# Kernel tuning notes

Measured on AMD Instinct MI355X. Metric: run time of the kernel, lower is better.

The kernel has to match this reference:

```python
import jax, jax.numpy as jnp
import numpy as np

NUM_GROUPS = 32
EPS = 1e-5


def group_norm(x, scale, bias):
    # x: [B, C, L], normalize per (group, batch) over (C//G, L)
    B, C, L = x.shape
    G = NUM_GROUPS
    xg = x.reshape(B, G, C // G, L)
    mean = xg.mean(axis=(2, 3), keepdims=True)
    var = xg.var(axis=(2, 3), keepdims=True)
    xg = (xg - mean) * jax.lax.rsqrt(var + EPS)
    h = xg.reshape(B, C, L)
    return h * scale[None, :, None] + bias[None, :, None]


def setup_inputs() -> dict:
    key = jax.random.key(0)
    ks = jax.random.split(key, 8)
    B, C, L = 8, 512, 2048
    s = 1.0 / np.sqrt(C)
    return {
        "x": jax.random.normal(ks[0], (B, C, L), jnp.float32),
        "gn_scale": jnp.ones((C,), jnp.float32),
        "gn_bias": jnp.zeros((C,), jnp.float32),
        "wq": jax.random.normal(ks[1], (C, C), jnp.float32) * s,
        "bq": jnp.zeros((C,), jnp.float32),
        "wk": jax.random.normal(ks[2], (C, C), jnp.float32) * s,
        "bk": jnp.zeros((C,), jnp.float32),
        "wv": jax.random.normal(ks[3], (C, C), jnp.float32) * s,
        "bv": jnp.zeros((C,), jnp.float32),
        "wo": jax.random.normal(ks[4], (C, C), jnp.float32) * s,
        "bo": jnp.zeros((C,), jnp.float32),
    }


def reference(x, gn_scale, gn_bias, wq, bq, wk, bk, wv, bv, wo, bo):
    B, C, L = x.shape
    h = group_norm(x, gn_scale, gn_bias)  # [B, C, L]
    # 1x1 conv == per-position linear; produce [B, L, C] directly
    q = jnp.einsum('oc,bcl->blo', wq, h) + bq
    k = jnp.einsum('oc,bcl->blo', wk, h) + bk
    v = jnp.einsum('oc,bcl->blo', wv, h) + bv
    scale = jnp.asarray(C, x.dtype) ** -0.5
    w = jnp.einsum('bqc,bkc->bqk', q, k) * scale  # [B, L, L]
    w = jax.nn.softmax(w, axis=-1)
    a = jnp.einsum('bqk,bkc->bqc', w, v)  # [B, L, C]
    out = jnp.einsum('oc,blc->bol', wo, a) + bo[None, :, None]  # [B, C, L]
    return x + out
```

## Files before the change

kernel.cpp:

```cpp
#include <hip/hip_runtime.h>

typedef __attribute__((ext_vector_type(8))) _Float16 half8;
typedef __attribute__((ext_vector_type(4))) _Float16 half4;
typedef __attribute__((ext_vector_type(4))) float floatx4;

#define AS1 __attribute__((address_space(1)))
#define AS3 __attribute__((address_space(3)))

__device__ __forceinline__ void async_load16(const void* g, void* l) {
  __builtin_amdgcn_global_load_lds((AS1 void*)(unsigned long long)g,
                                   (AS3 void*)(unsigned long long)l, 16, 0, 0);
}

template <int N>
__device__ __forceinline__ void wait_vm() {
  static_assert(N >= 0 && N <= 12, "extend wait_vm");
  if constexpr (N == 0) asm volatile("s_waitcnt vmcnt(0)" ::: "memory");
  else if constexpr (N == 1) asm volatile("s_waitcnt vmcnt(1)" ::: "memory");
  else if constexpr (N == 2) asm volatile("s_waitcnt vmcnt(2)" ::: "memory");
  else if constexpr (N == 3) asm volatile("s_waitcnt vmcnt(3)" ::: "memory");
  else if constexpr (N == 4) asm volatile("s_waitcnt vmcnt(4)" ::: "memory");
  else if constexpr (N == 5) asm volatile("s_waitcnt vmcnt(5)" ::: "memory");
  else if constexpr (N == 6) asm volatile("s_waitcnt vmcnt(6)" ::: "memory");
  else if constexpr (N == 7) asm volatile("s_waitcnt vmcnt(7)" ::: "memory");
  else if constexpr (N == 8) asm volatile("s_waitcnt vmcnt(8)" ::: "memory");
  else if constexpr (N == 9) asm volatile("s_waitcnt vmcnt(9)" ::: "memory");
  else if constexpr (N == 10) asm volatile("s_waitcnt vmcnt(10)" ::: "memory");
  else if constexpr (N == 11) asm volatile("s_waitcnt vmcnt(11)" ::: "memory");
  else asm volatile("s_waitcnt vmcnt(12)" ::: "memory");
}

__global__ __launch_bounds__(256) void gn_fused(const float* __restrict__ x,
                                                const float* __restrict__ gsc,
                                                const float* __restrict__ gbi,
                                                _Float16* __restrict__ ht) {
  constexpr int STR = 2056;
  __shared__ _Float16 xl[16 * STR];
  __shared__ float rs[4], rss[4], mv[2], scs[16], ofs[16];
  const int bg = blockIdx.x;
  const int b = bg >> 5, g = bg & 31;
  const float4* p4 = (const float4*)(x + (long long)bg * 32768);
  const int t = threadIdx.x;
  float s = 0.f, ss = 0.f;
  for (int i = t; i < 8192; i += 256) {
    float4 v = p4[i];
    const int c = i >> 9, lq = (i & 511) << 2;
    half4 pk;
    pk[0] = (_Float16)v.x; pk[1] = (_Float16)v.y;
    pk[2] = (_Float16)v.z; pk[3] = (_Float16)v.w;
    *(half4*)&xl[c * STR + lq] = pk;
    s += v.x + v.y + v.z + v.w;
    ss += v.x * v.x + v.y * v.y + v.z * v.z + v.w * v.w;
  }
#pragma unroll
  for (int off = 32; off; off >>= 1) { s += __shfl_down(s, off); ss += __shfl_down(ss, off); }
  if ((t & 63) == 0) { rs[t >> 6] = s; rss[t >> 6] = ss; }
  __syncthreads();
  if (t == 0) {
    s = rs[0] + rs[1] + rs[2] + rs[3];
    ss = rss[0] + rss[1] + rss[2] + rss[3];
    float mean = s * (1.f / 32768.f);
    float var = ss * (1.f / 32768.f) - mean * mean;
    mv[0] = mean; mv[1] = rsqrtf(var + 1e-5f);
  }
  __syncthreads();
  if (t < 16) {
    const float sc = gsc[g * 16 + t] * mv[1];
    scs[t] = sc;
    ofs[t] = gbi[g * 16 + t] - mv[0] * sc;
  }
  __syncthreads();
  const int l0 = t * 8;
  half8 hv[16];
#pragma unroll
  for (int c = 0; c < 16; ++c) hv[c] = *(const half8*)&xl[c * STR + l0];
  _Float16* dst0 = ht + ((long long)(b * 2048 + l0)) * 512 + g * 16;
#pragma unroll
  for (int j = 0; j < 8; ++j) {
    half8 o0, o1;
#pragma unroll
    for (int c = 0; c < 8; ++c) o0[c] = (_Float16)((float)hv[c][j] * scs[c] + ofs[c]);
#pragma unroll
    for (int c = 0; c < 8; ++c) o1[c] = (_Float16)((float)hv[c + 8][j] * scs[c + 8] + ofs[c + 8]);
    _Float16* dst = dst0 + (long long)j * 512;
    *(half8*)dst = o0;
    *(half8*)(dst + 8) = o1;
  }
}

__global__ __launch_bounds__(256) void cast_w(const float* __restrict__ w0, const float* __restrict__ w1,
                                              const float* __restrict__ w2, const float* __restrict__ w3,
                                              const float* __restrict__ bq, const float* __restrict__ bk,
                                              _Float16* __restrict__ outw, float* __restrict__ bqk) {
  const long long i = (long long)blockIdx.x * 256 + threadIdx.x;
  if (blockIdx.x < 4096) {
    const int m = (int)(i >> 18);
    const int r = (int)(i & 262143);
    const float* w = (m == 0) ? w0 : (m == 1) ? w1 : (m == 2) ? w2 : w3;
    outw[i] = (_Float16)w[r];
  } else {
    const int j = (int)(i - 4096LL * 256);
    bqk[j] = (j < 512) ? bq[j] : bk[j - 512];
  }
}

template <int BM, int BN, int BIAS_MODE , int OUT_TYPE , bool RESIDUAL>
__global__ __launch_bounds__(512, 2) void gemm2p(
    const _Float16* __restrict__ A, long long sA, int lda,
    const _Float16* __restrict__ Bt, long long sB, int ldb,
    void* __restrict__ Cv, long long sC, int ldc,
    const float* __restrict__ bias,
    const float* __restrict__ resid, long long sR,
    float alpha, int K) {
  constexpr int ASZ = BM * 64, BSZ = BN * 64;
  constexpr int BUF = ASZ + BSZ;
  constexpr int RWA = BM / 16, RWB = BN / 16;
  constexpr int LA = RWA / 8, LB = RWB / 8;
  constexpr int L = 2 * LA + 2 * LB;
  constexpr int NMI = BM / 64, NNJ = BN / 128;
  __shared__ __align__(16) _Float16 ls[2 * BUF];

  const int tid = threadIdx.x;
  const int wave = tid >> 6, lane = tid & 63;
  const int wr = wave >> 2, wc = wave & 3;
  const int fm = lane & 15, q = lane >> 4;
  const int bz = blockIdx.x;
  const int m0 = blockIdx.y * BM, n0 = blockIdx.z * BN;
  A += (long long)bz * sA;
  Bt += (long long)bz * sB;

  const int srow = lane >> 3;
  const int schunk = ((lane & 7) ^ (srow & 7)) * 8;
  const _Float16* pA0 = A + (long long)(m0 + RWA * wave + srow) * lda + schunk;
  const _Float16* pA1 = pA0 + (long long)(BM / 2) * lda;
  const _Float16* pB0 = Bt + (long long)(n0 + RWB * wave + srow) * ldb + schunk;
  const _Float16* pB1 = pB0 + (long long)(BN / 2) * ldb;
  const int dA0 = RWA * wave * 64;
  const int dB0 = ASZ + RWB * wave * 64;

  const int c0 = (q ^ (fm & 7)) * 8;
  const int c1 = ((q + 4) ^ (fm & 7)) * 8;
  const int arow = wr * (BM / 4) + fm;
  const int brow = wc * (BN / 8) + fm;

  floatx4 acc[2][2][NMI][NNJ] = {};
  half8 af[NMI][2], bf0[NNJ][2], bf1[NNJ][2];

  const int NT = K >> 6;

  {
    _Float16* st = ls;
#pragma unroll
    for (int s = 0; s < LA; ++s) async_load16(pA0 + (long long)(8 * s) * lda, st + dA0 + s * 512);
#pragma unroll
    for (int s = 0; s < LB; ++s) async_load16(pB0 + (long long)(8 * s) * ldb, st + dB0 + s * 512);
#pragma unroll
    for (int s = 0; s < LB; ++s) async_load16(pB1 + (long long)(8 * s) * ldb, st + dB0 + BSZ / 2 + s * 512);
#pragma unroll
    for (int s = 0; s < LA; ++s) async_load16(pA1 + (long long)(8 * s) * lda, st + dA0 + ASZ / 2 + s * 512);
    pA0 += 64; pA1 += 64; pB0 += 64; pB1 += 64;
    wait_vm<0>();
  }

#define G8_READ_A(MH)                                                      \
  _Pragma("unroll") for (int mi = 0; mi < NMI; ++mi) {                     \
    const int r_ = (MH) * (BM / 2) + arow + 16 * mi;                       \
    af[mi][0] = *(const half8*)&cb[r_ * 64 + c0];                          \
    af[mi][1] = *(const half8*)&cb[r_ * 64 + c1];                          \
  }
#define G8_READ_B(NH, BF)                                                  \
  _Pragma("unroll") for (int nj = 0; nj < NNJ; ++nj) {                     \
    const int r_ = ASZ + ((NH) * (BN / 2) + brow + 16 * nj) * 64;          \
    BF[nj][0] = *(const half8*)&cb[r_ + c0];                               \
    BF[nj][1] = *(const half8*)&cb[r_ + c1];                               \
  }
#define G8_MFMA(MH, NH, BF)                                                \
  __builtin_amdgcn_s_setprio(1);                                           \
  _Pragma("unroll") for (int kk = 0; kk < 2; ++kk)                         \
  _Pragma("unroll") for (int mi = 0; mi < NMI; ++mi)                       \
  _Pragma("unroll") for (int nj = 0; nj < NNJ; ++nj)                       \
    acc[MH][NH][mi][nj] = __builtin_amdgcn_mfma_f32_16x16x32_f16(          \
        af[mi][kk], BF[nj][kk], acc[MH][NH][mi][nj], 0, 0, 0);             \
  __builtin_amdgcn_s_setprio(0);
#define G8_STAGE_A(PTR, OFF)                                               \
  _Pragma("unroll") for (int s = 0; s < LA; ++s)                           \
    async_load16(PTR + (long long)(8 * s) * lda, st + dA0 + (OFF) + s * 512);
#define G8_STAGE_B(PTR, OFF)                                               \
  _Pragma("unroll") for (int s = 0; s < LB; ++s)                           \
    async_load16(PTR + (long long)(8 * s) * ldb, st + dB0 + (OFF) + s * 512);

  for (int kt = 0; kt < NT - 1; ++kt) {
    const _Float16* cb = ls + (kt & 1) * BUF;
    _Float16* st = ls + ((kt + 1) & 1) * BUF;
    __builtin_amdgcn_s_barrier();
    G8_READ_A(0)
    G8_READ_B(0, bf0)
    G8_READ_B(1, bf1)
    G8_STAGE_A(pA0, 0)
    G8_STAGE_B(pB0, 0)
    G8_STAGE_B(pB1, BSZ / 2)
    G8_STAGE_A(pA1, ASZ / 2)
    pA0 += 64; pA1 += 64; pB0 += 64; pB1 += 64;
    wait_vm<L>();
    G8_MFMA(0, 0, bf0)
    G8_MFMA(0, 1, bf1)
    __builtin_amdgcn_s_barrier();
    G8_READ_A(1)
    wait_vm<LA>();
    G8_MFMA(1, 1, bf1)
    G8_MFMA(1, 0, bf0)
  }
  {
    const _Float16* cb = ls + ((NT - 1) & 1) * BUF;
    __builtin_amdgcn_s_barrier();
    G8_READ_A(0)
    G8_READ_B(0, bf0)
    G8_READ_B(1, bf1)
    wait_vm<0>();
    G8_MFMA(0, 0, bf0)
    G8_MFMA(0, 1, bf1)
    __builtin_amdgcn_s_barrier();
    G8_READ_A(1)
    G8_MFMA(1, 1, bf1)
    G8_MFMA(1, 0, bf0)
  }

#undef G8_READ_A
#undef G8_READ_B
#undef G8_MFMA
#undef G8_STAGE_A
#undef G8_STAGE_B

#pragma unroll
  for (int mh = 0; mh < 2; ++mh)
#pragma unroll
    for (int nh = 0; nh < 2; ++nh)
#pragma unroll
      for (int mi = 0; mi < NMI; ++mi)
#pragma unroll
        for (int nj = 0; nj < NNJ; ++nj) {
          const int rr0 = m0 + mh * (BM / 2) + wr * (BM / 4) + 16 * mi + 4 * q;
          const int cc = n0 + nh * (BN / 2) + wc * (BN / 8) + 16 * nj + fm;
#pragma unroll
          for (int t = 0; t < 4; ++t) {
            const int rr = rr0 + t;
            float v = acc[mh][nh][mi][nj][t] * alpha;
            if (BIAS_MODE == 1) v += bias[cc];
            if (BIAS_MODE == 2) v += bias[rr];
            if (RESIDUAL) v += resid[(long long)bz * sR + (long long)rr * ldc + cc];
            const long long off = (long long)bz * sC + (long long)rr * ldc + cc;
            if (OUT_TYPE == 0) ((float*)Cv)[off] = v;
            else ((_Float16*)Cv)[off] = (_Float16)v;
          }
        }
}

__global__ __launch_bounds__(256) void row_stats(const _Float16* __restrict__ S,
                                                 float2* __restrict__ rms) {
  const int row = blockIdx.x * 4 + (threadIdx.x >> 6);
  const int lane = threadIdx.x & 63;
  const float4* p4 = (const float4*)(S + (long long)row * 2048);
  union U { float4 f; _Float16 h[8]; } u[4];
#pragma unroll
  for (int j = 0; j < 4; ++j) u[j].f = p4[lane + 64 * j];
  float v[32];
  float mx = -3e38f;
#pragma unroll
  for (int j = 0; j < 4; ++j)
#pragma unroll
    for (int i = 0; i < 8; ++i) { v[j * 8 + i] = (float)u[j].h[i]; mx = fmaxf(mx, v[j * 8 + i]); }
#pragma unroll
  for (int off = 32; off; off >>= 1) mx = fmaxf(mx, __shfl_xor(mx, off));
  float s = 0.f;
#pragma unroll
  for (int i = 0; i < 32; ++i) s += __expf(v[i] - mx);
#pragma unroll
  for (int off = 32; off; off >>= 1) s += __shfl_xor(s, off);
  if (lane == 0) rms[row] = make_float2(mx, 1.f / s);
}

__global__ __launch_bounds__(512, 2) void gemm_pv(
    const _Float16* __restrict__ S, const float2* __restrict__ rms,
    const _Float16* __restrict__ Vt, _Float16* __restrict__ Out) {
  constexpr int BM = 128, BN = 256;
  constexpr int ASZ = BM * 64, BSZ = BN * 64, BUF = ASZ + BSZ;
  constexpr int LB = 2;
  constexpr int NMI = 2, NNJ = 2;
  constexpr int NT = 32;
  __shared__ __align__(16) _Float16 ls[2 * BUF];

  const int tid = threadIdx.x;
  const int wave = tid >> 6, lane = tid & 63;
  const int wr = wave >> 2, wc = wave & 3;
  const int fm = lane & 15, q = lane >> 4;
  const int bz = blockIdx.x;
  const int m0 = blockIdx.y * BM, n0 = blockIdx.z * BN;

  const int srow = lane >> 3;
  const int schunk = ((lane & 7) ^ (srow & 7)) * 8;
  const int rA0 = m0 + 8 * wave + srow;
  const float2 st0 = rms[bz * 2048 + rA0];
  const float2 st1 = rms[bz * 2048 + rA0 + 64];
  const _Float16* pA0 = S + (long long)bz * 4194304 + (long long)rA0 * 2048 + schunk;
  const _Float16* pA1 = pA0 + 64LL * 2048;
  const _Float16* pB0 = Vt + (long long)bz * 1048576 + (long long)(n0 + 16 * wave + srow) * 2048 + schunk;
  const _Float16* pB1 = pB0 + 128LL * 2048;
  const int dA0 = 8 * wave * 64;
  const int dB0 = ASZ + 16 * wave * 64;

  const int c0 = (q ^ (fm & 7)) * 8;
  const int c1 = ((q + 4) ^ (fm & 7)) * 8;
  const int arow = wr * (BM / 4) + fm;
  const int brow = wc * (BN / 8) + fm;

  floatx4 acc[2][2][NMI][NNJ] = {};
  half8 afx[2][NMI][2], bfx[2][NNJ][2];

#define PV_EXPW(DST, RA, MM, INV)                                          \
  { half8 pe_;                                                             \
    _Pragma("unroll") for (int e = 0; e < 8; ++e)                          \
      pe_[e] = (_Float16)(__expf((float)(RA)[e] - (MM)) * (INV));          \
    *(half8*)(DST) = pe_; }
#define PV_DMA_B(PTR, OFF)                                                 \
  _Pragma("unroll") for (int s = 0; s < LB; ++s)                           \
    async_load16(PTR + (long long)(8 * s) * 2048, stb + dB0 + (OFF) + s * 512);

  {
    _Float16* stb = ls;
    half8 ra0 = *(const half8*)pA0;
    half8 ra1 = *(const half8*)pA1;
    PV_DMA_B(pB0, 0)
    PV_DMA_B(pB1, BSZ / 2)
    PV_EXPW(&stb[dA0 + lane * 8], ra0, st0.x, st0.y)
    PV_EXPW(&stb[dA0 + ASZ / 2 + lane * 8], ra1, st1.x, st1.y)
    pA0 += 64; pA1 += 64; pB0 += 64; pB1 += 64;
    asm volatile("s_waitcnt vmcnt(0) lgkmcnt(0)" ::: "memory");
  }

  for (int kt = 0; kt < NT; ++kt) {
    const _Float16* cb = ls + (kt & 1) * BUF;
    _Float16* stb = ls + ((kt + 1) & 1) * BUF;
    __builtin_amdgcn_s_barrier();
#pragma unroll
    for (int mh = 0; mh < 2; ++mh)
#pragma unroll
      for (int mi = 0; mi < NMI; ++mi) {
        const int r_ = mh * (BM / 2) + arow + 16 * mi;
        afx[mh][mi][0] = *(const half8*)&cb[r_ * 64 + c0];
        afx[mh][mi][1] = *(const half8*)&cb[r_ * 64 + c1];
      }
#pragma unroll
    for (int nh = 0; nh < 2; ++nh)
#pragma unroll
      for (int nj = 0; nj < NNJ; ++nj) {
        const int r_ = ASZ + (nh * (BN / 2) + brow + 16 * nj) * 64;
        bfx[nh][nj][0] = *(const half8*)&cb[r_ + c0];
        bfx[nh][nj][1] = *(const half8*)&cb[r_ + c1];
      }
    half8 ra0, ra1;
    const bool more = (kt < NT - 1);
    if (more) {
      ra0 = *(const half8*)pA0;
      ra1 = *(const half8*)pA1;
      PV_DMA_B(pB0, 0)
      PV_DMA_B(pB1, BSZ / 2)
      pB0 += 64; pB1 += 64;
    }
    __builtin_amdgcn_s_setprio(1);
#pragma unroll
    for (int kk = 0; kk < 2; ++kk)
#pragma unroll
      for (int mh = 0; mh < 2; ++mh)
#pragma unroll
        for (int mi = 0; mi < NMI; ++mi)
#pragma unroll
          for (int nh = 0; nh < 2; ++nh)
#pragma unroll
            for (int nj = 0; nj < NNJ; ++nj)
              acc[mh][nh][mi][nj] = __builtin_amdgcn_mfma_f32_16x16x32_f16(
                  afx[mh][mi][kk], bfx[nh][nj][kk], acc[mh][nh][mi][nj], 0, 0, 0);
    __builtin_amdgcn_s_setprio(0);
    if (more) {
      PV_EXPW(&stb[dA0 + lane * 8], ra0, st0.x, st0.y)
      PV_EXPW(&stb[dA0 + ASZ / 2 + lane * 8], ra1, st1.x, st1.y)
      pA0 += 64; pA1 += 64;
    }
    asm volatile("s_waitcnt vmcnt(0) lgkmcnt(0)" ::: "memory");
  }
#undef PV_EXPW
#undef PV_DMA_B

#pragma unroll
  for (int mh = 0; mh < 2; ++mh)
#pragma unroll
    for (int nh = 0; nh < 2; ++nh)
#pragma unroll
      for (int mi = 0; mi < NMI; ++mi)
#pragma unroll
        for (int nj = 0; nj < NNJ; ++nj) {
          const int rr0 = m0 + mh * (BM / 2) + wr * (BM / 4) + 16 * mi + 4 * q;
          const int cc = n0 + nh * (BN / 2) + wc * (BN / 8) + 16 * nj + fm;
#pragma unroll
          for (int t = 0; t < 4; ++t) {
            const int rr = rr0 + t;
            Out[(long long)bz * 1048576 + (long long)rr * 512 + cc] =
                (_Float16)acc[mh][nh][mi][nj][t];
          }
        }
}

extern "C" void kernel_launch(void* const* d_in, const int* in_sizes, int n_in,
                              void* d_out, int out_size, void* d_ws, size_t ws_size,
                              hipStream_t stream) {
  const float* x = (const float*)d_in[0];
  const float* gsc = (const float*)d_in[1];
  const float* gbi = (const float*)d_in[2];
  const float* wq = (const float*)d_in[3];
  const float* bq = (const float*)d_in[4];
  const float* wk = (const float*)d_in[5];
  const float* bk = (const float*)d_in[6];
  const float* wv = (const float*)d_in[7];
  const float* bv = (const float*)d_in[8];
  const float* wo = (const float*)d_in[9];
  const float* bo = (const float*)d_in[10];
  float* out = (float*)d_out;

  char* ws = (char*)d_ws;
  float* bqk = (float*)(ws + 2048);
  _Float16* wbf = (_Float16*)(ws + 8192);
  _Float16* ht = wbf + 4 * 262144;
  const long long EB = 8LL * 2048 * 512;
  _Float16* qk = ht + EB;
  _Float16* vm = qk + 2 * EB;
  _Float16* Sb = vm + EB;
  _Float16* at = ht;
  float2* rms = (float2*)qk;

  gn_fused<<<256, 256, 0, stream>>>(x, gsc, gbi, ht);
  cast_w<<<4100, 256, 0, stream>>>(wq, wk, wv, wo, bq, bk, wbf, bqk);

  const float scale = 0.044194173824159216f;
  gemm2p<256, 256, 1, 1, false><<<dim3(8, 8, 4), 512, 0, stream>>>(
      ht, 1048576LL, 512, wbf, 0LL, 512, qk, 2097152LL, 1024, bqk, nullptr, 0LL, 1.f, 512);
  gemm2p<128, 256, 2, 1, false><<<dim3(8, 4, 8), 512, 0, stream>>>(
      wbf + 2 * 262144, 0LL, 512, ht, 1048576LL, 512, vm, 1048576LL, 2048, bv, nullptr, 0LL, 1.f, 512);
  gemm2p<256, 256, 0, 1, false><<<dim3(8, 8, 8), 512, 0, stream>>>(
      qk, 2097152LL, 1024, qk + 512, 2097152LL, 1024, Sb, 4194304LL, 2048, nullptr, nullptr, 0LL, scale, 512);
  row_stats<<<4096, 256, 0, stream>>>(Sb, rms);
  gemm_pv<<<dim3(8, 16, 2), 512, 0, stream>>>(Sb, rms, vm, at);
  gemm2p<128, 256, 2, 0, true><<<dim3(8, 4, 8), 512, 0, stream>>>(
      wbf + 3 * 262144, 0LL, 512, at, 1048576LL, 512, out, 1048576LL, 2048, bo, x, 1048576LL, 1.f, 512);
}
```

Before: 284.4 us.

## Merge prep kernels and fuse QK and V projections into one launch

Folds the group-norm kernel and the weight/bias cast kernel into a single prep launch, with extra blocks handling the casts. The QK projection and the V projection are merged into one grouped GEMM launch of 384 blocks, where each block picks its operands by index, and the V part now uses 256x256 tiles instead of 128x256. This removes launch overhead and tail gaps between small kernels and fills the GPU better. The cost is a runtime branch for bias mode, and the prep blocks inherit the large shared-memory allocation, which may limit how many cast blocks fit at once.

```diff
diff --git a/kernel.cpp b/kernel.cpp
--- a/kernel.cpp
+++ b/kernel.cpp
@@ -30,17 +30,34 @@
   else asm volatile("s_waitcnt vmcnt(12)" ::: "memory");
 }
 
-__global__ __launch_bounds__(256) void gn_fused(const float* __restrict__ x,
-                                                const float* __restrict__ gsc,
-                                                const float* __restrict__ gbi,
-                                                _Float16* __restrict__ ht) {
+__global__ __launch_bounds__(256) void prep(
+    const float* __restrict__ x, const float* __restrict__ gsc, const float* __restrict__ gbi,
+    _Float16* __restrict__ ht,
+    const float* __restrict__ w0, const float* __restrict__ w1,
+    const float* __restrict__ w2, const float* __restrict__ w3,
+    const float* __restrict__ bq, const float* __restrict__ bk,
+    _Float16* __restrict__ outw, float* __restrict__ bqk) {
   constexpr int STR = 2056;
   __shared__ _Float16 xl[16 * STR];
   __shared__ float rs[4], rss[4], mv[2], scs[16], ofs[16];
+  const int t = threadIdx.x;
+  if (blockIdx.x >= 256) {
+    const int cb = blockIdx.x - 256;
+    const long long i = (long long)cb * 256 + t;
+    if (cb < 4096) {
+      const int m = (int)(i >> 18);
+      const int r = (int)(i & 262143);
+      const float* w = (m == 0) ? w0 : (m == 1) ? w1 : (m == 2) ? w2 : w3;
+      outw[i] = (_Float16)w[r];
+    } else {
+      const int j = (int)(i - 4096LL * 256);
+      bqk[j] = (j < 512) ? bq[j] : bk[j - 512];
+    }
+    return;
+  }
   const int bg = blockIdx.x;
   const int b = bg >> 5, g = bg & 31;
   const float4* p4 = (const float4*)(x + (long long)bg * 32768);
-  const int t = threadIdx.x;
   float s = 0.f, ss = 0.f;
   for (int i = t; i < 8192; i += 256) {
     float4 v = p4[i];
@@ -88,46 +105,25 @@
   }
 }
 
-__global__ __launch_bounds__(256) void cast_w(const float* __restrict__ w0, const float* __restrict__ w1,
-                                              const float* __restrict__ w2, const float* __restrict__ w3,
-                                              const float* __restrict__ bq, const float* __restrict__ bk,
-                                              _Float16* __restrict__ outw, float* __restrict__ bqk) {
-  const long long i = (long long)blockIdx.x * 256 + threadIdx.x;
-  if (blockIdx.x < 4096) {
-    const int m = (int)(i >> 18);
-    const int r = (int)(i & 262143);
-    const float* w = (m == 0) ? w0 : (m == 1) ? w1 : (m == 2) ? w2 : w3;
-    outw[i] = (_Float16)w[r];
-  } else {
-    const int j = (int)(i - 4096LL * 256);
-    bqk[j] = (j < 512) ? bq[j] : bk[j - 512];
-  }
-}
-
-template <int BM, int BN, int BIAS_MODE , int OUT_TYPE , bool RESIDUAL>
-__global__ __launch_bounds__(512, 2) void gemm2p(
-    const _Float16* __restrict__ A, long long sA, int lda,
-    const _Float16* __restrict__ Bt, long long sB, int ldb,
-    void* __restrict__ Cv, long long sC, int ldc,
-    const float* __restrict__ bias,
-    const float* __restrict__ resid, long long sR,
-    float alpha, int K) {
+template <int BM, int BN, int OUT_TYPE , bool RESIDUAL>
+__device__ __forceinline__ void gemm_body(
+    const _Float16* __restrict__ A, int lda,
+    const _Float16* __restrict__ Bt, int ldb,
+    void* __restrict__ Cv, int ldc,
+    const float* __restrict__ bias, int bias_mode,
+    const float* __restrict__ resid,
+    float alpha, int K, int m0, int n0, _Float16* ls) {
   constexpr int ASZ = BM * 64, BSZ = BN * 64;
   constexpr int BUF = ASZ + BSZ;
   constexpr int RWA = BM / 16, RWB = BN / 16;
   constexpr int LA = RWA / 8, LB = RWB / 8;
   constexpr int L = 2 * LA + 2 * LB;
   constexpr int NMI = BM / 64, NNJ = BN / 128;
-  __shared__ __align__(16) _Float16 ls[2 * BUF];
 
   const int tid = threadIdx.x;
   const int wave = tid >> 6, lane = tid & 63;
   const int wr = wave >> 2, wc = wave & 3;
   const int fm = lane & 15, q = lane >> 4;
-  const int bz = blockIdx.x;
-  const int m0 = blockIdx.y * BM, n0 = blockIdx.z * BN;
-  A += (long long)bz * sA;
-  Bt += (long long)bz * sB;
 
   const int srow = lane >> 3;
   const int schunk = ((lane & 7) ^ (srow & 7)) * 8;
@@ -245,14 +241,61 @@
           for (int t = 0; t < 4; ++t) {
             const int rr = rr0 + t;
             float v = acc[mh][nh][mi][nj][t] * alpha;
-            if (BIAS_MODE == 1) v += bias[cc];
-            if (BIAS_MODE == 2) v += bias[rr];
-            if (RESIDUAL) v += resid[(long long)bz * sR + (long long)rr * ldc + cc];
-            const long long off = (long long)bz * sC + (long long)rr * ldc + cc;
+            if (bias) v += (bias_mode == 1) ? bias[cc] : bias[rr];
+            if (RESIDUAL) v += resid[(long long)rr * ldc + cc];
+            const long long off = (long long)rr * ldc + cc;
             if (OUT_TYPE == 0) ((float*)Cv)[off] = v;
             else ((_Float16*)Cv)[off] = (_Float16)v;
           }
         }
+}
+
+template <int BM, int BN, int OUT_TYPE, bool RESIDUAL>
+__global__ __launch_bounds__(512, 2) void gemm2p(
+    const _Float16* __restrict__ A, long long sA, int lda,
+    const _Float16* __restrict__ Bt, long long sB, int ldb,
+    void* __restrict__ Cv, long long sC, int ldc,
+    const float* __restrict__ bias, int bias_mode,
+    const float* __restrict__ resid, long long sR,
+    float alpha, int K) {
+  __shared__ __align__(16) _Float16 ls[2 * (BM + BN) * 64];
+  const int bz = blockIdx.x;
+  void* C = (OUT_TYPE == 0) ? (void*)((float*)Cv + (long long)bz * sC)
+                            : (void*)((_Float16*)Cv + (long long)bz * sC);
+  gemm_body<BM, BN, OUT_TYPE, RESIDUAL>(
+      A + (long long)bz * sA, lda, Bt + (long long)bz * sB, ldb, C, ldc,
+      bias, bias_mode, RESIDUAL ? resid + (long long)bz * sR : nullptr,
+      alpha, K, blockIdx.y * BM, blockIdx.z * BN, ls);
+}
+
+__global__ __launch_bounds__(512, 2) void gemm_qkv(
+    const _Float16* __restrict__ ht, const _Float16* __restrict__ wqk,
+    const _Float16* __restrict__ wv,
+    _Float16* __restrict__ qk, _Float16* __restrict__ vm,
+    const float* __restrict__ bqk, const float* __restrict__ bv) {
+  __shared__ __align__(16) _Float16 ls[2 * 512 * 64];
+  const int gi = blockIdx.x;
+  const int bz = gi & 7, ti = gi >> 3;
+  const _Float16 *Ab, *Bb;
+  _Float16* Cb;
+  const float* bb;
+  int ldc, bmode, m0, n0;
+  if (ti < 32) {
+    Ab = ht + (long long)bz * 1048576;
+    Bb = wqk;
+    Cb = qk + (long long)bz * 2097152;
+    ldc = 1024; bb = bqk; bmode = 1;
+    m0 = (ti >> 2) * 256; n0 = (ti & 3) * 256;
+  } else {
+    const int t2 = ti - 32;
+    Ab = wv;
+    Bb = ht + (long long)bz * 1048576;
+    Cb = vm + (long long)bz * 1048576;
+    ldc = 2048; bb = bv; bmode = 2;
+    m0 = (t2 >> 3) * 256; n0 = (t2 & 7) * 256;
+  }
+  gemm_body<256, 256, 1, false>(Ab, 512, Bb, 512, Cb, ldc, bb, bmode, nullptr,
+                                1.f, 512, m0, n0, ls);
 }
 
 __global__ __launch_bounds__(256) void row_stats(const _Float16* __restrict__ S,
@@ -436,18 +479,16 @@
   _Float16* at = ht;
   float2* rms = (float2*)qk;
 
-  gn_fused<<<256, 256, 0, stream>>>(x, gsc, gbi, ht);
-  cast_w<<<4100, 256, 0, stream>>>(wq, wk, wv, wo, bq, bk, wbf, bqk);
+  prep<<<4356, 256, 0, stream>>>(x, gsc, gbi, ht, wq, wk, wv, wo, bq, bk, wbf, bqk);
 
   const float scale = 0.044194173824159216f;
-  gemm2p<256, 256, 1, 1, false><<<dim3(8, 8, 4), 512, 0, stream>>>(
-      ht, 1048576LL, 512, wbf, 0LL, 512, qk, 2097152LL, 1024, bqk, nullptr, 0LL, 1.f, 512);
-  gemm2p<128, 256, 2, 1, false><<<dim3(8, 4, 8), 512, 0, stream>>>(
-      wbf + 2 * 262144, 0LL, 512, ht, 1048576LL, 512, vm, 1048576LL, 2048, bv, nullptr, 0LL, 1.f, 512);
-  gemm2p<256, 256, 0, 1, false><<<dim3(8, 8, 8), 512, 0, stream>>>(
-      qk, 2097152LL, 1024, qk + 512, 2097152LL, 1024, Sb, 4194304LL, 2048, nullptr, nullptr, 0LL, scale, 512);
+  gemm_qkv<<<384, 512, 0, stream>>>(ht, wbf, wbf + 2 * 262144, qk, vm, bqk, bv);
+  gemm2p<256, 256, 1, false><<<dim3(8, 8, 8), 512, 0, stream>>>(
+      qk, 2097152LL, 1024, qk + 512, 2097152LL, 1024, Sb, 4194304LL, 2048,
+      nullptr, 0, nullptr, 0LL, scale, 512);
   row_stats<<<4096, 256, 0, stream>>>(Sb, rms);
   gemm_pv<<<dim3(8, 16, 2), 512, 0, stream>>>(Sb, rms, vm, at);
-  gemm2p<128, 256, 2, 0, true><<<dim3(8, 4, 8), 512, 0, stream>>>(
-      wbf + 3 * 262144, 0LL, 512, at, 1048576LL, 512, out, 1048576LL, 2048, bo, x, 1048576LL, 1.f, 512);
-}
+  gemm2p<128, 256, 0, true><<<dim3(8, 4, 8), 512, 0, stream>>>(
+      wbf + 3 * 262144, 0LL, 512, at, 1048576LL, 512, out, 1048576LL, 2048,
+      bo, 2, x, 1048576LL, 1.f, 512);
+}
```

Result: slower. 326.6 us (+14.8%).
